# Kernel optimization log

Hardware: AMD Instinct MI355X
Metric: run time of the kernel (lower is better)

Reference implementation:

```python
import jax, jax.numpy as jnp
import numpy as np

NEG_SLOPE = 0.2  # LeakyReLU slope in GAT attention
HEADS = 10

def gat_layer(x, src, dst, W, a_src, a_dst, b, H, C, N):
    # x: [N, F_in]; W: [F_in, H*C]; a_src/a_dst: [H, C]; b: [C]
    h = (x @ W).reshape(N, H, C)                      # [N, H, C]
    e_s = (h * a_src).sum(-1)                         # [N, H]
    e_d = (h * a_dst).sum(-1)                         # [N, H]
    e = jax.nn.leaky_relu(e_s[src] + e_d[dst], NEG_SLOPE)  # [E, H]
    m = jax.ops.segment_max(e, dst, num_segments=N)
    m = jnp.where(jnp.isfinite(m), m, 0.0)
    p = jnp.exp(e - m[dst])                           # [E, H]
    denom = jax.ops.segment_sum(p, dst, num_segments=N)
    alpha = p / (denom[dst] + 1e-16)                  # [E, H]
    out = jax.ops.segment_sum(alpha[:, :, None] * h[src], dst, num_segments=N)  # [N, H, C]
    return out.mean(1) + b                            # heads averaged (concat=False)


def setup_inputs() -> dict:
    key = jax.random.key(0)
    N, E, F, CLS = 10000, 160000, 24, 24
    ks = jax.random.split(key, 24)
    p = lambda k, shp: 0.1 * jax.random.normal(k, shp, dtype=jnp.float32)
    return {
        "x": jax.random.normal(ks[0], (N, F), dtype=jnp.float32),
        "edge_index": jax.random.randint(ks[1], (2, E), 0, N, dtype=jnp.int64),
        "batch": jnp.sort(jax.random.randint(ks[2], (N,), 0, 64, dtype=jnp.int64)),
        "W0": p(ks[3], (F, 16)), "b0": p(ks[4], (16,)),
        "Wc1": p(ks[5], (16, HEADS * 32)), "as1": p(ks[6], (HEADS, 32)), "ad1": p(ks[7], (HEADS, 32)), "bc1": p(ks[8], (32,)),
        "Wc2": p(ks[9], (32, HEADS * 64)), "as2": p(ks[10], (HEADS, 64)), "ad2": p(ks[11], (HEADS, 64)), "bc2": p(ks[12], (64,)),
        "Wc3": p(ks[13], (64, HEADS * 128)), "as3": p(ks[14], (HEADS, 128)), "ad3": p(ks[15], (HEADS, 128)), "bc3": p(ks[16], (128,)),
        "W1": p(ks[17], (128, 256)), "b1": p(ks[18], (256,)),
        "W2": p(ks[19], (256, CLS)), "b2": p(ks[20], (CLS,)),
    }


def reference(x, edge_index, batch, W0, b0, Wc1, as1, ad1, bc1, Wc2, as2, ad2, bc2,
              Wc3, as3, ad3, bc3, W1, b1, W2, b2):
    N = x.shape[0]
    self_loop = jnp.arange(N, dtype=edge_index.dtype)
    src = jnp.concatenate([edge_index[0], self_loop])
    dst = jnp.concatenate([edge_index[1], self_loop])
    h = jax.nn.elu(x @ W0 + b0)
    h = jax.nn.elu(gat_layer(h, src, dst, Wc1, as1, ad1, bc1, HEADS, 32, N))
    h = jax.nn.elu(gat_layer(h, src, dst, Wc2, as2, ad2, bc2, HEADS, 64, N))
    h = jax.nn.elu(gat_layer(h, src, dst, Wc3, as3, ad3, bc3, HEADS, 128, N))
    h = jax.nn.elu(h @ W1 + b1)
    # dropout is identity in eval mode
    logits = h @ W2 + b2
    return jax.nn.log_softmax(logits, axis=1)
```

## Files before the change

### kernel.cpp

```cpp
#include <hip/hip_runtime.h>
#include <hip/hip_bf16.h>
#include <math.h>

#define NHEADS 10

typedef unsigned short ushort_t;
typedef unsigned int uint_t;

typedef __attribute__((ext_vector_type(4))) float f32x4;
typedef __attribute__((ext_vector_type(8))) short short8;

__device__ __forceinline__ float bu2f(ushort_t u){ return __uint_as_float(((uint_t)u)<<16); }
__device__ __forceinline__ ushort_t f2bu(float f){
    uint_t b = __float_as_uint(f);
    return (ushort_t)((b + 0x7FFFu + ((b>>16)&1u)) >> 16);
}

__global__ void k_scan(int* cnt, int N, int ET, int* indptr){
    __shared__ int lds[1024];
    int t = threadIdx.x;
    int chunk = (N + 1023)/1024;
    int base = t*chunk;
    int s = 0;
    for(int i=0;i<chunk;i++){ int idx=base+i; if(idx<N) s += cnt[idx]; }
    lds[t]=s;
    __syncthreads();
    for(int off=1; off<1024; off<<=1){
        int v = (t>=off)? lds[t-off] : 0;
        __syncthreads();
        lds[t]+=v;
        __syncthreads();
    }
    int run = lds[t]-s;
    for(int i=0;i<chunk;i++){
        int idx=base+i;
        if(idx<N){
            int c = cnt[idx];
            indptr[idx]=run;
            cnt[idx]=run;
            run += c;
        }
    }
    if(t==0) indptr[N]=ET;
}

__global__ void k_fill(const int* eidx, int E, int N, int* cursor, int* srcs){
    int e = blockIdx.x*blockDim.x + threadIdx.x;
    int ET = E + N;
    if(e >= ET) return;
    int s, d;
    if(e < E){ s = eidx[e]; d = eidx[E+e]; } else { s = e-E; d = e-E; }
    int pos = atomicAdd(&cursor[d], 1);
    srcs[pos] = s;
}

__global__ void k_sortw(const int* indptr, int* srcs, int N){
    int wid  = (blockIdx.x*blockDim.x + threadIdx.x) >> 6;
    int lane = threadIdx.x & 63;
    if(wid >= N) return;
    int p0 = indptr[wid], p1 = indptr[wid+1];
    int deg = p1 - p0;
    if(deg <= 1) return;
    if(deg <= 64){
        int v = (lane < deg) ? srcs[p0+lane] : 0x7FFFFFFF;
        #pragma unroll
        for(int k=2; k<=64; k<<=1){
            #pragma unroll
            for(int j=k>>1; j>0; j>>=1){
                int partner = __shfl_xor(v, j, 64);
                bool dir   = ((lane & k) == 0);
                bool small = ((lane & j) == 0);
                int mn = min(v, partner), mx = max(v, partner);
                v = (dir == small) ? mn : mx;
            }
        }
        if(lane < deg) srcs[p0+lane] = v;
    } else if(lane == 0){
        for(int i=p0+1;i<p1;i++){
            int v2 = srcs[i]; int j=i-1;
            while(j>=p0 && srcs[j]>v2){ srcs[j+1]=srcs[j]; j--; }
            srcs[j+1]=v2;
        }
    }
}

__global__ void k_setup(const float* __restrict__ W1c,const float* __restrict__ W2c,
                        const float* __restrict__ W3c,const float* __restrict__ W4c,
                        ushort_t* T1,ushort_t* T2,ushort_t* T3,ushort_t* T4,
                        const float* __restrict__ x, const float* __restrict__ W0,
                        const float* __restrict__ b0, float* __restrict__ fc0o,
                        const int* __restrict__ eidx, int* cnt, int E, int N){
    int idx = blockIdx.x*blockDim.x + threadIdx.x;
    if(idx < 10240){ int c=idx/32, k=idx%32; T1[idx] = (k<16)? f2bu(W1c[(size_t)k*320+c]) : (ushort_t)0; return; }
    idx -= 10240;
    if(idx < 20480){ int c=idx/32, k=idx%32; T2[idx] = f2bu(W2c[(size_t)k*640+c]); return; }
    idx -= 20480;
    if(idx < 81920){ int c=idx/64, k=idx%64; T3[idx] = f2bu(W3c[(size_t)k*1280+c]); return; }
    idx -= 81920;
    if(idx < 32768){ int c=idx/128, k=idx%128; T4[idx] = f2bu(W4c[(size_t)k*256+c]); return; }
    idx -= 32768;
    if(idx < N*16){
        int n = idx>>4, c = idx&15;
        float acc = b0[c];
        #pragma unroll
        for(int k=0;k<24;k++) acc += x[n*24+k] * W0[k*16+c];
        fc0o[idx] = acc>0.f ? acc : expm1f(acc);
        return;
    }
    idx -= N*16;
    if(idx < E+N){
        int d = (idx < E) ? eidx[E + idx] : (idx - E);
        atomicAdd(&cnt[d], 1);
    }
}

template<int K, int KP, int EPI, int OUTBF16, int HPT>
__global__ void __launch_bounds__(256, 4)
k_gemm(const float* __restrict__ A, const ushort_t* __restrict__ BT,
       const float* __restrict__ bias, void* __restrict__ Cmat,
       int N, int HC,
       const float* __restrict__ a_s, const float* __restrict__ a_d,
       float* __restrict__ es, float* __restrict__ ed){
    int t = threadIdx.x;
    int w = t >> 6, lane = t & 63;
    int lr = lane & 15, lk = lane >> 4;
    int row0 = blockIdx.x*64, col0 = blockIdx.y*64;
    int row = row0 + w*16 + lr;

    f32x4 acc[4];
    #pragma unroll
    for(int f=0; f<4; f++) acc[f] = (f32x4){0.f,0.f,0.f,0.f};

    #pragma unroll
    for(int kb = 0; kb < K; kb += 32){
        int k0 = kb + lk*8;
        short8 af = {0,0,0,0,0,0,0,0};
        if(row < N && k0 < K){
            const float* ap = &A[(size_t)row*K + k0];
            float4 a0 = *(const float4*)ap;
            float4 a1 = *(const float4*)(ap + 4);
            af[0]=(short)f2bu(a0.x); af[1]=(short)f2bu(a0.y);
            af[2]=(short)f2bu(a0.z); af[3]=(short)f2bu(a0.w);
            af[4]=(short)f2bu(a1.x); af[5]=(short)f2bu(a1.y);
            af[6]=(short)f2bu(a1.z); af[7]=(short)f2bu(a1.w);
        }
        #pragma unroll
        for(int f=0; f<4; f++){
            int col = col0 + f*16 + lr;
            short8 bf = *(const short8*)&BT[(size_t)col*KP + k0];
            acc[f] = __builtin_amdgcn_mfma_f32_16x16x32_bf16(af, bf, acc[f], 0, 0, 0);
        }
    }

    #pragma unroll
    for(int f=0; f<4; f++){
        #pragma unroll
        for(int j=0; j<4; j++){
            int r = row0 + w*16 + lk*4 + j;
            if(r >= N) continue;
            int col = col0 + f*16 + lr;
            float v = acc[f][j];
            if(EPI){
                v += bias[col];
                v = v>0.f ? v : expm1f(v);
            }
            if(OUTBF16) ((ushort_t*)Cmat)[(size_t)r*HC + col] = f2bu(v);
            else        ((float*)Cmat)[(size_t)r*HC + col] = v;
        }
    }

    if constexpr (HPT > 0){
        constexpr int CH = 64/HPT;
        #pragma unroll
        for(int j=0; j<4; j++){
            int r = row0 + w*16 + lk*4 + j;
            float sp[HPT], dp[HPT];
            #pragma unroll
            for(int g=0; g<HPT; g++){ sp[g]=0.f; dp[g]=0.f; }
            #pragma unroll
            for(int f=0; f<4; f++){
                float vb = bu2f(f2bu(acc[f][j]));
                int g   = (HPT==2) ? (f>>1) : 0;
                int cih = (HPT==2) ? ((f&1)*16 + lr) : (f*16 + lr);
                int ai  = col0 + g*CH + cih;
                sp[g] += vb * a_s[ai];
                dp[g] += vb * a_d[ai];
            }
            #pragma unroll
            for(int st=1; st<16; st<<=1){
                #pragma unroll
                for(int g=0; g<HPT; g++){
                    sp[g] += __shfl_xor(sp[g], st, 64);
                    dp[g] += __shfl_xor(dp[g], st, 64);
                }
            }
            if(lr == 0 && r < N){
                #pragma unroll
                for(int g=0; g<HPT; g++){
                    int head = col0/CH + g;
                    es[r*NHEADS + head] = sp[g];
                    ed[r*NHEADS + head] = dp[g];
                }
            }
        }
    }
}

template<int C>
__global__ void k_attn(const ushort_t* hf, const float* a_s, const float* a_d,
                       float* es, float* ed, int N){
    int tid = blockIdx.x*blockDim.x + threadIdx.x;
    if(tid >= N*NHEADS*4) return;
    int q   = tid & 3;
    int idx = tid >> 2;
    int n = idx/NHEADS, h = idx%NHEADS;
    constexpr int CQ = C/4;
    const ushort_t* hp = hf + (size_t)n*NHEADS*C + h*C + q*CQ;
    const float* asp = a_s + h*C + q*CQ;
    const float* adp = a_d + h*C + q*CQ;
    float s=0.f, d=0.f;
    #pragma unroll
    for(int cb=0; cb<CQ/8; cb++){
        uint4 qv = *(const uint4*)(hp + cb*8);
        uint_t uu[4] = {qv.x, qv.y, qv.z, qv.w};
        #pragma unroll
        for(int j=0;j<4;j++){
            float f0 = __uint_as_float(uu[j]<<16);
            float f1 = __uint_as_float(uu[j] & 0xFFFF0000u);
            int c = cb*8 + j*2;
            s += f0*asp[c] + f1*asp[c+1];
            d += f0*adp[c] + f1*adp[c+1];
        }
    }
    s += __shfl_xor(s, 1, 64); s += __shfl_xor(s, 2, 64);
    d += __shfl_xor(d, 1, 64); d += __shfl_xor(d, 2, 64);
    if(q == 0){ es[idx]=s; ed[idx]=d; }
}

template<int C>
__global__ void __launch_bounds__(256, 4)
k_fused(const int* __restrict__ indptr, const int* __restrict__ srcs,
        const float* __restrict__ es, const float* __restrict__ ed,
        const ushort_t* __restrict__ hf, const float* __restrict__ bc,
        float* __restrict__ out, int N)
{
    __shared__ float wlds[4][64*NHEADS];
    __shared__ float stat[4][NHEADS];
    __shared__ int   degs[4];
    int wslot = threadIdx.x >> 6;
    int lane  = threadIdx.x & 63;
    int n = (blockIdx.x << 2) + wslot;
    bool valid = (n < N);
    int p0 = 0, deg = 0;
    if(valid){ p0 = indptr[n]; deg = indptr[n+1] - p0; }
    if(lane == 0) degs[wslot] = deg;
    __syncthreads();
    int maxdeg = max(max(degs[0],degs[1]), max(degs[2],degs[3]));
    int nch = (maxdeg + 63) >> 6;
    float* wl = wlds[wslot];

    int e6 = lane/10, h6 = lane%10;
    float edv = (valid && lane < 60) ? ed[n*NHEADS + h6] : 0.f;

    float denp = 0.f;
    for(int c = 0; c < nch; c++){
        int base = c << 6;
        int lim = deg - base; if(lim > 64) lim = 64; if(lim < 0) lim = 0;
        if(valid && lane < 60){
            for(int i = e6; i < lim; i += 6){
                float v = es[(size_t)srcs[p0+base+i]*NHEADS + h6] + edv;
                v = (v >= 0.f) ? v : 0.2f*v;
                float wv = expf(fminf(v, 60.f));
                wl[i*NHEADS + h6] = wv;
                denp += wv;
            }
        }
        __syncthreads();
    }
    float tA = __shfl(denp, lane+30, 64);
    if(lane < 30) denp += tA;
    float tB = __shfl(denp, lane+10, 64);
    float tC = __shfl(denp, lane+20, 64);
    if(lane < 10) denp += tB + tC;
    if(valid && lane < NHEADS) stat[wslot][lane] = 1.f/(denp + 1e-30f);
    __syncthreads();

    constexpr int TPN = C/8;
    constexpr int EG  = 64/TPN;
    int local = lane % TPN, eg = lane / TPN;
    int c8 = local*8;
    float dinv_r[NHEADS];
    #pragma unroll
    for(int h=0; h<NHEADS; h++) dinv_r[h] = stat[wslot][h];
    float acc[8];
    #pragma unroll
    for(int i=0;i<8;i++) acc[i]=0.f;

    for(int c = 0; c < nch; c++){
        int base = c << 6;
        int lim = deg - base; if(lim > 64) lim = 64; if(lim < 0) lim = 0;
        if(nch > 1){
            if(valid && lane < 60){
                for(int i = e6; i < lim; i += 6){
                    float v = es[(size_t)srcs[p0+base+i]*NHEADS + h6] + edv;
                    v = (v >= 0.f) ? v : 0.2f*v;
                    wl[i*NHEADS + h6] = expf(fminf(v, 60.f));
                }
            }
            __syncthreads();
        }
        if(valid){
            for(int i = eg; i < lim; i += EG){
                int s = srcs[p0+base+i];
                const ushort_t* hp = hf + (size_t)s*NHEADS*C + c8;
                const float* wp = &wl[i*NHEADS];
                #pragma unroll
                for(int h=0;h<NHEADS;h++){
                    uint4 q = *(const uint4*)(hp + h*C);
                    float wd = wp[h]*dinv_r[h];
                    acc[0] += wd * __uint_as_float(q.x<<16);
                    acc[1] += wd * __uint_as_float(q.x & 0xFFFF0000u);
                    acc[2] += wd * __uint_as_float(q.y<<16);
                    acc[3] += wd * __uint_as_float(q.y & 0xFFFF0000u);
                    acc[4] += wd * __uint_as_float(q.z<<16);
                    acc[5] += wd * __uint_as_float(q.z & 0xFFFF0000u);
                    acc[6] += wd * __uint_as_float(q.w<<16);
                    acc[7] += wd * __uint_as_float(q.w & 0xFFFF0000u);
                }
            }
        }
        if(nch > 1) __syncthreads();
    }

    #pragma unroll
    for(int s = TPN; s < 64; s <<= 1){
        #pragma unroll
        for(int i=0;i<8;i++) acc[i] += __shfl_xor(acc[i], s, 64);
    }
    if(valid && eg == 0){
        float4 v0, v1;
        #pragma unroll
        for(int i=0;i<8;i++){
            float v = acc[i]*(1.f/NHEADS) + bc[c8+i];
            v = v>0.f ? v : expm1f(v);
            if(i<4) ((float*)&v0)[i] = v; else ((float*)&v1)[i-4] = v;
        }
        *(float4*)&out[(size_t)n*C + c8]     = v0;
        *(float4*)&out[(size_t)n*C + c8 + 4] = v1;
    }
}

__global__ void k_head(const float* hin, const float* W2, const float* b2v, float* out, int N){
    int grp  = threadIdx.x/32;
    int lane = threadIdx.x%32;
    int n = blockIdx.x*8 + grp;
    if(n>=N) return;
    float acc = -1e30f;
    if(lane < 24){
        acc = b2v[lane];
        for(int k=0;k<256;k++) acc += hin[n*256+k]*W2[k*24+lane];
    }
    float mx = acc;
    for(int off=16; off; off>>=1) mx = fmaxf(mx, __shfl_xor(mx, off, 32));
    float ex = (lane<24)? expf(acc-mx) : 0.f;
    float sm = ex;
    for(int off=16; off; off>>=1) sm += __shfl_xor(sm, off, 32);
    if(lane<24) out[n*24+lane] = acc - mx - logf(sm);
}

extern "C" void kernel_launch(void* const* d_in, const int* in_sizes, int n_in,
                              void* d_out, int out_size, void* d_ws, size_t ws_size,
                              hipStream_t stream) {
    const float* x   = (const float*)d_in[0];
    const int*  eidx = (const int*)d_in[1];
    const float* W0 = (const float*)d_in[3];  const float* b0 = (const float*)d_in[4];
    const float* Wc1= (const float*)d_in[5];  const float* as1= (const float*)d_in[6];
    const float* ad1= (const float*)d_in[7];  const float* bc1= (const float*)d_in[8];
    const float* Wc2= (const float*)d_in[9];  const float* as2= (const float*)d_in[10];
    const float* ad2= (const float*)d_in[11]; const float* bc2= (const float*)d_in[12];
    const float* Wc3= (const float*)d_in[13]; const float* as3= (const float*)d_in[14];
    const float* ad3= (const float*)d_in[15]; const float* bc3= (const float*)d_in[16];
    const float* W1 = (const float*)d_in[17]; const float* b1 = (const float*)d_in[18];
    const float* W2 = (const float*)d_in[19]; const float* b2 = (const float*)d_in[20];
    float* out = (float*)d_out;

    const int N  = in_sizes[0]/24;
    const int E  = in_sizes[1]/2;
    const int ET = E + N;

    char* w = (char*)d_ws;
    size_t off = 0;
    auto alloc = [&](size_t bytes)->void* {
        void* p = w + off;
        off = (off + bytes + 255) & ~(size_t)255;
        return p;
    };
    int*   cnt    = (int*)  alloc((size_t)N*4);
    int*   indptr = (int*)  alloc((size_t)(N+1)*4);
    int*   srcs   = (int*)  alloc((size_t)ET*4);
    float* es     = (float*)alloc((size_t)N*NHEADS*4);
    float* ed     = (float*)alloc((size_t)N*NHEADS*4);
    float* nfA    = (float*)alloc((size_t)N*256*4);
    float* nfB    = (float*)alloc((size_t)N*256*4);
    ushort_t* hf  = (ushort_t*)alloc((size_t)N*1280*2);
    ushort_t* WT1 = (ushort_t*)alloc((size_t)320*32*2);
    ushort_t* WT2 = (ushort_t*)alloc((size_t)640*32*2);
    ushort_t* WT3 = (ushort_t*)alloc((size_t)1280*64*2);
    ushort_t* WT4 = (ushort_t*)alloc((size_t)256*128*2);

    hipMemsetAsync(cnt, 0, (size_t)N*4, stream);
    int setupWork = 145408 + N*16 + ET;
    k_setup<<<(setupWork+255)/256,256,0,stream>>>(Wc1, Wc2, Wc3, W1, WT1, WT2, WT3, WT4,
                                                  x, W0, b0, nfA, eidx, cnt, E, N);
    k_scan <<<1,1024,0,stream>>>(cnt, N, ET, indptr);
    int gE = (ET+255)/256;
    k_fill <<<gE,256,0,stream>>>(eidx, E, N, cnt, srcs);
    k_sortw<<<((size_t)N*64+255)/256,256,0,stream>>>(indptr, srcs, N);

    int gRow = (N+63)/64;
    int gNode = (N+3)/4;
    int gA   = (N*NHEADS*4+255)/256;

    k_gemm<16,32,0,1,2><<<dim3(gRow,320/64),256,0,stream>>>(nfA, WT1, nullptr, hf, N, 320, as1, ad1, es, ed);
    k_fused<32><<<gNode,256,0,stream>>>(indptr, srcs, es, ed, hf, bc1, nfB, N);

    k_gemm<32,32,0,1,1><<<dim3(gRow,640/64),256,0,stream>>>(nfB, WT2, nullptr, hf, N, 640, as2, ad2, es, ed);
    k_fused<64><<<gNode,256,0,stream>>>(indptr, srcs, es, ed, hf, bc2, nfA, N);

    k_gemm<64,64,0,1,0><<<dim3(gRow,1280/64),256,0,stream>>>(nfA, WT3, nullptr, hf, N, 1280, nullptr, nullptr, nullptr, nullptr);
    k_attn<128><<<gA,256,0,stream>>>(hf, as3, ad3, es, ed, N);
    k_fused<128><<<gNode,256,0,stream>>>(indptr, srcs, es, ed, hf, bc3, nfB, N);

    k_gemm<128,128,1,0,0><<<dim3(gRow,256/64),256,0,stream>>>(nfB, WT4, b1, nfA, N, 256, nullptr, nullptr, nullptr, nullptr);
    k_head<<<(N+7)/8,256,0,stream>>>(nfA, W2, b2, out, N);
}
```

Before: 285.9 us.

## Stage source indices in LDS and double-buffer feature gathers for single-chunk nodes

Caches each node's first 64 source indices in shared memory so the logit and aggregation passes stop re-reading them from global memory. For nodes that fit in one chunk, the attention weights are pre-normalised in LDS, and the aggregation loop is software-pipelined with two register buffers so the next edge's 10-head bf16 feature gather is issued while the current one is accumulated. The two extra uint4[10] buffers raise register pressure, which could reduce occupancy under launch_bounds(256,4). An extra block-wide barrier is added.

```diff
diff --git a/kernel.cpp b/kernel.cpp
--- a/kernel.cpp
+++ b/kernel.cpp
@@ -246,6 +246,7 @@
 {
     __shared__ float wlds[4][64*NHEADS];
     __shared__ float stat[4][NHEADS];
+    __shared__ int   slds4[4][64];
     __shared__ int   degs[4];
     int wslot = threadIdx.x >> 6;
     int lane  = threadIdx.x & 63;
@@ -254,10 +255,12 @@
     int p0 = 0, deg = 0;
     if(valid){ p0 = indptr[n]; deg = indptr[n+1] - p0; }
     if(lane == 0) degs[wslot] = deg;
+    if(valid && lane < deg && lane < 64) slds4[wslot][lane] = srcs[p0+lane];
     __syncthreads();
     int maxdeg = max(max(degs[0],degs[1]), max(degs[2],degs[3]));
     int nch = (maxdeg + 63) >> 6;
     float* wl = wlds[wslot];
+    const int* sl = slds4[wslot];
 
     int e6 = lane/10, h6 = lane%10;
     float edv = (valid && lane < 60) ? ed[n*NHEADS + h6] : 0.f;
@@ -268,7 +271,8 @@
         int lim = deg - base; if(lim > 64) lim = 64; if(lim < 0) lim = 0;
         if(valid && lane < 60){
             for(int i = e6; i < lim; i += 6){
-                float v = es[(size_t)srcs[p0+base+i]*NHEADS + h6] + edv;
+                int sv = (c == 0) ? sl[i] : srcs[p0+base+i];
+                float v = es[(size_t)sv*NHEADS + h6] + edv;
                 v = (v >= 0.f) ? v : 0.2f*v;
                 float wv = expf(fminf(v, 60.f));
                 wl[i*NHEADS + h6] = wv;
@@ -284,22 +288,65 @@
     if(lane < 10) denp += tB + tC;
     if(valid && lane < NHEADS) stat[wslot][lane] = 1.f/(denp + 1e-30f);
     __syncthreads();
+    if(nch == 1 && valid && lane < 60){
+        float dv = stat[wslot][h6];
+        for(int i = e6; i < deg; i += 6) wl[i*NHEADS + h6] *= dv;
+    }
+    __syncthreads();
 
     constexpr int TPN = C/8;
     constexpr int EG  = 64/TPN;
     int local = lane % TPN, eg = lane / TPN;
     int c8 = local*8;
-    float dinv_r[NHEADS];
-    #pragma unroll
-    for(int h=0; h<NHEADS; h++) dinv_r[h] = stat[wslot][h];
     float acc[8];
     #pragma unroll
     for(int i=0;i<8;i++) acc[i]=0.f;
 
-    for(int c = 0; c < nch; c++){
-        int base = c << 6;
-        int lim = deg - base; if(lim > 64) lim = 64; if(lim < 0) lim = 0;
-        if(nch > 1){
+    if(nch == 1){
+        int lim = deg;
+        uint4 qA[NHEADS], qB[NHEADS];
+        auto loadQ = [&](uint4* q, int idx){
+            const ushort_t* hp = hf + (size_t)sl[idx]*NHEADS*C + c8;
+            #pragma unroll
+            for(int h=0;h<NHEADS;h++) q[h] = *(const uint4*)(hp + h*C);
+        };
+        auto consume = [&](uint4* q, int idx){
+            const float* wp = &wl[idx*NHEADS];
+            #pragma unroll
+            for(int h=0;h<NHEADS;h++){
+                float wd = wp[h];
+                acc[0] += wd * __uint_as_float(q[h].x<<16);
+                acc[1] += wd * __uint_as_float(q[h].x & 0xFFFF0000u);
+                acc[2] += wd * __uint_as_float(q[h].y<<16);
+                acc[3] += wd * __uint_as_float(q[h].y & 0xFFFF0000u);
+                acc[4] += wd * __uint_as_float(q[h].z<<16);
+                acc[5] += wd * __uint_as_float(q[h].z & 0xFFFF0000u);
+                acc[6] += wd * __uint_as_float(q[h].w<<16);
+                acc[7] += wd * __uint_as_float(q[h].w & 0xFFFF0000u);
+            }
+        };
+        int i = eg;
+        if(i < lim){
+            loadQ(qA, i);
+            while(true){
+                int j = i + EG;
+                if(j < lim) loadQ(qB, j);
+                consume(qA, i);
+                if(j >= lim) break;
+                int k2 = j + EG;
+                if(k2 < lim) loadQ(qA, k2);
+                consume(qB, j);
+                if(k2 >= lim) break;
+                i = k2;
+            }
+        }
+    } else {
+        float dinv_r[NHEADS];
+        #pragma unroll
+        for(int h=0; h<NHEADS; h++) dinv_r[h] = stat[wslot][h];
+        for(int c = 0; c < nch; c++){
+            int base = c << 6;
+            int lim = deg - base; if(lim > 64) lim = 64; if(lim < 0) lim = 0;
             if(valid && lane < 60){
                 for(int i = e6; i < lim; i += 6){
                     float v = es[(size_t)srcs[p0+base+i]*NHEADS + h6] + edv;
@@ -308,28 +355,28 @@
                 }
             }
             __syncthreads();
-        }
-        if(valid){
-            for(int i = eg; i < lim; i += EG){
-                int s = srcs[p0+base+i];
-                const ushort_t* hp = hf + (size_t)s*NHEADS*C + c8;
-                const float* wp = &wl[i*NHEADS];
-                #pragma unroll
-                for(int h=0;h<NHEADS;h++){
-                    uint4 q = *(const uint4*)(hp + h*C);
-                    float wd = wp[h]*dinv_r[h];
-                    acc[0] += wd * __uint_as_float(q.x<<16);
-                    acc[1] += wd * __uint_as_float(q.x & 0xFFFF0000u);
-                    acc[2] += wd * __uint_as_float(q.y<<16);
-                    acc[3] += wd * __uint_as_float(q.y & 0xFFFF0000u);
-                    acc[4] += wd * __uint_as_float(q.z<<16);
-                    acc[5] += wd * __uint_as_float(q.z & 0xFFFF0000u);
-                    acc[6] += wd * __uint_as_float(q.w<<16);
-                    acc[7] += wd * __uint_as_float(q.w & 0xFFFF0000u);
+            if(valid){
+                for(int i = eg; i < lim; i += EG){
+                    int s = srcs[p0+base+i];
+                    const ushort_t* hp = hf + (size_t)s*NHEADS*C + c8;
+                    const float* wp = &wl[i*NHEADS];
+                    #pragma unroll
+                    for(int h=0;h<NHEADS;h++){
+                        uint4 q = *(const uint4*)(hp + h*C);
+                        float wd = wp[h]*dinv_r[h];
+                        acc[0] += wd * __uint_as_float(q.x<<16);
+                        acc[1] += wd * __uint_as_float(q.x & 0xFFFF0000u);
+                        acc[2] += wd * __uint_as_float(q.y<<16);
+                        acc[3] += wd * __uint_as_float(q.y & 0xFFFF0000u);
+                        acc[4] += wd * __uint_as_float(q.z<<16);
+                        acc[5] += wd * __uint_as_float(q.z & 0xFFFF0000u);
+                        acc[6] += wd * __uint_as_float(q.w<<16);
+                        acc[7] += wd * __uint_as_float(q.w & 0xFFFF0000u);
+                    }
                 }
             }
-        }
-        if(nch > 1) __syncthreads();
+            __syncthreads();
+        }
     }
 
     #pragma unroll
```

Result: slower. 452.2 us (+58.2%).

## Fuse layer-3 attention dot products into GEMM epilogue and prescale weights

Applied to the files above, without the earlier changes.

Removes the separate k_attn kernel for the third GAT layer. The GEMM epilogue now computes per-head source and destination attention scores from the bf16-rounded outputs and accumulates them into es/ed with atomics, after two memsets zero those buffers. In the aggregation kernel, when a node fits in one 64-edge chunk, edge weights are normalised in LDS once, and the gather loop processes two heads per iteration without a per-head multiply. Atomics add nondeterministic summation order, plus two extra memset launches.

```diff
diff --git a/kernel.cpp b/kernel.cpp
--- a/kernel.cpp
+++ b/kernel.cpp
@@ -204,37 +204,30 @@
             }
         }
     }
-}
-
-template<int C>
-__global__ void k_attn(const ushort_t* hf, const float* a_s, const float* a_d,
-                       float* es, float* ed, int N){
-    int tid = blockIdx.x*blockDim.x + threadIdx.x;
-    if(tid >= N*NHEADS*4) return;
-    int q   = tid & 3;
-    int idx = tid >> 2;
-    int n = idx/NHEADS, h = idx%NHEADS;
-    constexpr int CQ = C/4;
-    const ushort_t* hp = hf + (size_t)n*NHEADS*C + h*C + q*CQ;
-    const float* asp = a_s + h*C + q*CQ;
-    const float* adp = a_d + h*C + q*CQ;
-    float s=0.f, d=0.f;
-    #pragma unroll
-    for(int cb=0; cb<CQ/8; cb++){
-        uint4 qv = *(const uint4*)(hp + cb*8);
-        uint_t uu[4] = {qv.x, qv.y, qv.z, qv.w};
-        #pragma unroll
-        for(int j=0;j<4;j++){
-            float f0 = __uint_as_float(uu[j]<<16);
-            float f1 = __uint_as_float(uu[j] & 0xFFFF0000u);
-            int c = cb*8 + j*2;
-            s += f0*asp[c] + f1*asp[c+1];
-            d += f0*adp[c] + f1*adp[c+1];
-        }
-    }
-    s += __shfl_xor(s, 1, 64); s += __shfl_xor(s, 2, 64);
-    d += __shfl_xor(d, 1, 64); d += __shfl_xor(d, 2, 64);
-    if(q == 0){ es[idx]=s; ed[idx]=d; }
+    if constexpr (HPT == -1){
+        int head = col0 >> 7;
+        #pragma unroll
+        for(int j=0; j<4; j++){
+            int r = row0 + w*16 + lk*4 + j;
+            float sp=0.f, dp=0.f;
+            #pragma unroll
+            for(int f=0; f<4; f++){
+                float vb = bu2f(f2bu(acc[f][j]));
+                int ai = (head<<7) + (col0 & 127) + f*16 + lr;
+                sp += vb * a_s[ai];
+                dp += vb * a_d[ai];
+            }
+            #pragma unroll
+            for(int st=1; st<16; st<<=1){
+                sp += __shfl_xor(sp, st, 64);
+                dp += __shfl_xor(dp, st, 64);
+            }
+            if(lr == 0 && r < N){
+                atomicAdd(&es[r*NHEADS + head], sp);
+                atomicAdd(&ed[r*NHEADS + head], dp);
+            }
+        }
+    }
 }
 
 template<int C>
@@ -284,22 +277,48 @@
     if(lane < 10) denp += tB + tC;
     if(valid && lane < NHEADS) stat[wslot][lane] = 1.f/(denp + 1e-30f);
     __syncthreads();
+    if(nch == 1 && valid && lane < 60){
+        float dv = stat[wslot][h6];
+        for(int i = e6; i < deg; i += 6) wl[i*NHEADS + h6] *= dv;
+    }
+    __syncthreads();
 
     constexpr int TPN = C/8;
     constexpr int EG  = 64/TPN;
     int local = lane % TPN, eg = lane / TPN;
     int c8 = local*8;
-    float dinv_r[NHEADS];
-    #pragma unroll
-    for(int h=0; h<NHEADS; h++) dinv_r[h] = stat[wslot][h];
     float acc[8];
     #pragma unroll
     for(int i=0;i<8;i++) acc[i]=0.f;
 
-    for(int c = 0; c < nch; c++){
-        int base = c << 6;
-        int lim = deg - base; if(lim > 64) lim = 64; if(lim < 0) lim = 0;
-        if(nch > 1){
+    if(nch == 1){
+        for(int i = eg; i < deg; i += EG){
+            int s = srcs[p0+i];
+            const ushort_t* hp = hf + (size_t)s*NHEADS*C + c8;
+            const float2* wp2 = (const float2*)&wl[i*NHEADS];
+            #pragma unroll
+            for(int hh=0; hh<5; hh++){
+                float2 wv = wp2[hh];
+                uint4 q0 = *(const uint4*)(hp + (2*hh)*C);
+                uint4 q1 = *(const uint4*)(hp + (2*hh+1)*C);
+                float w0 = wv.x, w1 = wv.y;
+                acc[0] += w0 * __uint_as_float(q0.x<<16) + w1 * __uint_as_float(q1.x<<16);
+                acc[1] += w0 * __uint_as_float(q0.x & 0xFFFF0000u) + w1 * __uint_as_float(q1.x & 0xFFFF0000u);
+                acc[2] += w0 * __uint_as_float(q0.y<<16) + w1 * __uint_as_float(q1.y<<16);
+                acc[3] += w0 * __uint_as_float(q0.y & 0xFFFF0000u) + w1 * __uint_as_float(q1.y & 0xFFFF0000u);
+                acc[4] += w0 * __uint_as_float(q0.z<<16) + w1 * __uint_as_float(q1.z<<16);
+                acc[5] += w0 * __uint_as_float(q0.z & 0xFFFF0000u) + w1 * __uint_as_float(q1.z & 0xFFFF0000u);
+                acc[6] += w0 * __uint_as_float(q0.w<<16) + w1 * __uint_as_float(q1.w<<16);
+                acc[7] += w0 * __uint_as_float(q0.w & 0xFFFF0000u) + w1 * __uint_as_float(q1.w & 0xFFFF0000u);
+            }
+        }
+    } else {
+        float dinv_r[NHEADS];
+        #pragma unroll
+        for(int h=0; h<NHEADS; h++) dinv_r[h] = stat[wslot][h];
+        for(int c = 0; c < nch; c++){
+            int base = c << 6;
+            int lim = deg - base; if(lim > 64) lim = 64; if(lim < 0) lim = 0;
             if(valid && lane < 60){
                 for(int i = e6; i < lim; i += 6){
                     float v = es[(size_t)srcs[p0+base+i]*NHEADS + h6] + edv;
@@ -308,28 +327,28 @@
                 }
             }
             __syncthreads();
-        }
-        if(valid){
-            for(int i = eg; i < lim; i += EG){
-                int s = srcs[p0+base+i];
-                const ushort_t* hp = hf + (size_t)s*NHEADS*C + c8;
-                const float* wp = &wl[i*NHEADS];
-                #pragma unroll
-                for(int h=0;h<NHEADS;h++){
-                    uint4 q = *(const uint4*)(hp + h*C);
-                    float wd = wp[h]*dinv_r[h];
-                    acc[0] += wd * __uint_as_float(q.x<<16);
-                    acc[1] += wd * __uint_as_float(q.x & 0xFFFF0000u);
-                    acc[2] += wd * __uint_as_float(q.y<<16);
-                    acc[3] += wd * __uint_as_float(q.y & 0xFFFF0000u);
-                    acc[4] += wd * __uint_as_float(q.z<<16);
-                    acc[5] += wd * __uint_as_float(q.z & 0xFFFF0000u);
-                    acc[6] += wd * __uint_as_float(q.w<<16);
-                    acc[7] += wd * __uint_as_float(q.w & 0xFFFF0000u);
+            if(valid){
+                for(int i = eg; i < lim; i += EG){
+                    int s = srcs[p0+base+i];
+                    const ushort_t* hp = hf + (size_t)s*NHEADS*C + c8;
+                    const float* wp = &wl[i*NHEADS];
+                    #pragma unroll
+                    for(int h=0;h<NHEADS;h++){
+                        uint4 q = *(const uint4*)(hp + h*C);
+                        float wd = wp[h]*dinv_r[h];
+                        acc[0] += wd * __uint_as_float(q.x<<16);
+                        acc[1] += wd * __uint_as_float(q.x & 0xFFFF0000u);
+                        acc[2] += wd * __uint_as_float(q.y<<16);
+                        acc[3] += wd * __uint_as_float(q.y & 0xFFFF0000u);
+                        acc[4] += wd * __uint_as_float(q.z<<16);
+                        acc[5] += wd * __uint_as_float(q.z & 0xFFFF0000u);
+                        acc[6] += wd * __uint_as_float(q.w<<16);
+                        acc[7] += wd * __uint_as_float(q.w & 0xFFFF0000u);
+                    }
                 }
             }
-        }
-        if(nch > 1) __syncthreads();
+            __syncthreads();
+        }
     }
 
     #pragma unroll
@@ -419,7 +438,6 @@
 
     int gRow = (N+63)/64;
     int gNode = (N+3)/4;
-    int gA   = (N*NHEADS*4+255)/256;
 
     k_gemm<16,32,0,1,2><<<dim3(gRow,320/64),256,0,stream>>>(nfA, WT1, nullptr, hf, N, 320, as1, ad1, es, ed);
     k_fused<32><<<gNode,256,0,stream>>>(indptr, srcs, es, ed, hf, bc1, nfB, N);
@@ -427,8 +445,9 @@
     k_gemm<32,32,0,1,1><<<dim3(gRow,640/64),256,0,stream>>>(nfB, WT2, nullptr, hf, N, 640, as2, ad2, es, ed);
     k_fused<64><<<gNode,256,0,stream>>>(indptr, srcs, es, ed, hf, bc2, nfA, N);
 
-    k_gemm<64,64,0,1,0><<<dim3(gRow,1280/64),256,0,stream>>>(nfA, WT3, nullptr, hf, N, 1280, nullptr, nullptr, nullptr, nullptr);
-    k_attn<128><<<gA,256,0,stream>>>(hf, as3, ad3, es, ed, N);
+    hipMemsetAsync(es, 0, (size_t)N*NHEADS*4, stream);
+    hipMemsetAsync(ed, 0, (size_t)N*NHEADS*4, stream);
+    k_gemm<64,64,0,1,-1><<<dim3(gRow,1280/64),256,0,stream>>>(nfA, WT3, nullptr, hf, N, 1280, as3, ad3, es, ed);
     k_fused<128><<<gNode,256,0,stream>>>(indptr, srcs, es, ed, hf, bc3, nfB, N);
 
     k_gemm<128,128,1,0,0><<<dim3(gRow,256/64),256,0,stream>>>(nfB, WT4, b1, nfA, N, 256, nullptr, nullptr, nullptr, nullptr);
```

After: 277.9 us. 1.03x faster.
